# Kernel tuning notes

Hardware: AMD Instinct MI355X
Metric: run time of the kernel (lower is better)

The kernel has to match this reference:

```python
import jax, jax.numpy as jnp
import numpy as np
import math

B, S, D, H = 2, 2048, 1024, 16
HD = D // H
KL_GAMMA = 0.1
EPS = 1e-10


def setup_inputs() -> dict:
    key = jax.random.key(0)
    ks = jax.random.split(key, 12)
    # positive inputs + positive weights keep scores > 0 so log(mean(scores)) is finite
    query = jax.random.uniform(ks[0], (B, S, D), dtype=jnp.float32)
    k_in = jax.random.uniform(ks[1], (B, S, D), dtype=jnp.float32)
    v_in = jax.random.uniform(ks[2], (B, S, D), dtype=jnp.float32)
    def w(k):
        return jax.random.uniform(k, (D, D), dtype=jnp.float32) * 0.002
    b = jnp.full((D,), 1e-3, dtype=jnp.float32)
    return {
        "query": query, "key": k_in, "value": v_in,
        "Wq": w(ks[3]), "bq": b,
        "Wk": w(ks[4]), "bk": b,
        "Wv": w(ks[5]), "bv": b,
        "Wo": w(ks[6]), "bo": b,
    }


def reference(query, key, value, Wq, bq, Wk, bk, Wv, bv, Wo, bo):
    Bq, Sq, _ = query.shape
    Sk = key.shape[1]
    # projections, split heads: [B, H, S, HD]
    Q = (query @ Wq + bq).reshape(Bq, Sq, H, HD).transpose(0, 2, 1, 3)
    K = (key @ Wk + bk).reshape(Bq, Sk, H, HD).transpose(0, 2, 1, 3)
    V = (value @ Wv + bv).reshape(Bq, Sk, H, HD).transpose(0, 2, 1, 3)
    scores = jnp.einsum("bhqd,bhkd->bhqk", Q, K) / math.sqrt(HD)  # [B,H,Sq,Sk]
    # KL bias: row-mean broadcast over keys, then log
    target = jnp.mean(scores, axis=-1, keepdims=True)  # [B,H,Sq,1]
    scores = scores + KL_GAMMA * jnp.log(target + EPS)
    attn = jax.nn.softmax(scores, axis=-1)
    ctx = jnp.einsum("bhqk,bhkd->bhqd", attn, V)
    ctx = ctx.transpose(0, 2, 1, 3).reshape(Bq, Sq, D)
    return ctx @ Wo + bo
```

## Files before the change

### kernel.cpp

```cpp
#include <hip/hip_runtime.h>
#include <hip/hip_bf16.h>
#include <stdint.h>


#define NB 2
#define NS 2048
#define ND 1024
#define NH 16
#define HD 64

typedef short bf16x8 __attribute__((ext_vector_type(8)));
typedef short bf16x4 __attribute__((ext_vector_type(4)));
typedef float f32x4 __attribute__((ext_vector_type(4)));
typedef float f32x16 __attribute__((ext_vector_type(16)));
typedef unsigned int u32x4 __attribute__((ext_vector_type(4)));

static __device__ __forceinline__ short f2bf(float f) {
    uint32_t u = __builtin_bit_cast(uint32_t, f);
    uint32_t r = (u + 0x7fffu + ((u >> 16) & 1u)) >> 16;
    return (short)(uint16_t)r;
}

static __device__ __forceinline__ unsigned int cvtpk(float lo, float hi) {
    unsigned int r;
    asm("v_cvt_pk_bf16_f32 %0, %1, %2" : "=v"(r) : "v"(lo), "v"(hi));
    return r;
}

#if __has_builtin(__builtin_amdgcn_exp2f)
#define EXP2(x) __builtin_amdgcn_exp2f(x)
#else
#define EXP2(x) exp2f(x)
#endif

static __device__ __forceinline__ void plswap(unsigned& a, unsigned& b) {
#if __has_builtin(__builtin_amdgcn_permlane32_swap)
    auto r = __builtin_amdgcn_permlane32_swap(a, b, false, false);
    a = r[0]; b = r[1];
#else
    const int l = (int)(threadIdx.x & 63);
    unsigned bl = __shfl(b, l & 31);
    unsigned ah = __shfl(a, (l & 31) + 32);
    a = (l < 32) ? a : bl;
    b = (l < 32) ? ah : b;
#endif
}

typedef __attribute__((address_space(1))) const unsigned int glob_u32;
typedef __attribute__((address_space(3))) unsigned int lds_u32;
static __device__ __forceinline__ void gload16(const void* g, void* l) {
    __builtin_amdgcn_global_load_lds((glob_u32*)g, (lds_u32*)l, 16, 0, 0);
}

__global__ __launch_bounds__(256) void prep_cast(const float* __restrict__ q,
                                                 const float* __restrict__ k,
                                                 const float* __restrict__ v,
                                                 short* __restrict__ Qo,
                                                 short* __restrict__ Ko,
                                                 short* __restrict__ Vo) {
    const float* src = (blockIdx.z == 0) ? q : (blockIdx.z == 1) ? k : v;
    short* dst = (blockIdx.z == 0) ? Qo : (blockIdx.z == 1) ? Ko : Vo;
    const size_t i = ((size_t)blockIdx.x * 256 + threadIdx.x) * 8;
    f32x4 a = *(const f32x4*)(src + i);
    f32x4 b = *(const f32x4*)(src + i + 4);
    bf16x8 o;
    o[0] = f2bf(a[0]); o[1] = f2bf(a[1]); o[2] = f2bf(a[2]); o[3] = f2bf(a[3]);
    o[4] = f2bf(b[0]); o[5] = f2bf(b[1]); o[6] = f2bf(b[2]); o[7] = f2bf(b[3]);
    *(bf16x8*)(dst + i) = o;
}

__global__ __launch_bounds__(256) void prep_wt(const float* __restrict__ W0,
                                               const float* __restrict__ W1,
                                               const float* __restrict__ W2,
                                               const float* __restrict__ W3,
                                               short* __restrict__ WtAll) {
    __shared__ short tile[32][33];
    const float* W = (blockIdx.z == 0) ? W0 : (blockIdx.z == 1) ? W1
                   : (blockIdx.z == 2) ? W2 : W3;
    short* Wt = WtAll + (size_t)blockIdx.z * (ND * ND);
    const int tx = threadIdx.x & 31;
    const int ty = threadIdx.x >> 5;
    const int k0 = blockIdx.x * 32, n0 = blockIdx.y * 32;
#pragma unroll
    for (int i = 0; i < 4; i++)
        tile[ty + i * 8][tx] = f2bf(W[(size_t)(k0 + ty + i * 8) * ND + n0 + tx]);
    __syncthreads();
#pragma unroll
    for (int i = 0; i < 4; i++)
        Wt[(size_t)(n0 + ty + i * 8) * ND + k0 + tx] = tile[tx][ty + i * 8];
}

static __device__ __forceinline__ void gemm_body(const short* __restrict__ A,
                                                 const short* __restrict__ Wt,
                                                 const float* __restrict__ bias,
                                                 void* __restrict__ Out,
                                                 int mode, float scale,
                                                 short* As, short* Bs) {
    const int tid = threadIdx.x;
    const int gm = blockIdx.x * 128;
    const int gn = blockIdx.y * 128;
    const int w = tid >> 6;
    const int l = tid & 63;
    const int r = l & 15;
    const int g = l >> 4;
    const int wr = w >> 1, wc = w & 1;

    f32x4 acc[4][4];
#pragma unroll
    for (int m = 0; m < 4; m++)
#pragma unroll
        for (int n = 0; n < 4; n++) acc[m][n] = (f32x4){0.f, 0.f, 0.f, 0.f};

    for (int k0 = 0; k0 < ND; k0 += 32) {
#pragma unroll
        for (int j = 0; j < 2; j++) {
            const int lin = ((w * 2 + j) << 10) + l * 16;
            const int row = lin >> 6;
            const int cb = lin & 63;
            gload16((const char*)A + ((size_t)(gm + row) * ND + k0) * 2 + cb,
                    (char*)As + ((w * 2 + j) << 10));
            gload16((const char*)Wt + ((size_t)(gn + row) * ND + k0) * 2 + cb,
                    (char*)Bs + ((w * 2 + j) << 10));
        }
        __syncthreads();

        bf16x8 af[4], bfv[4];
#pragma unroll
        for (int m = 0; m < 4; m++)
            af[m] = *(const bf16x8*)((const char*)As + (wr * 64 + m * 16 + r) * 64 + g * 16);
#pragma unroll
        for (int n = 0; n < 4; n++)
            bfv[n] = *(const bf16x8*)((const char*)Bs + (wc * 64 + n * 16 + r) * 64 + g * 16);
#pragma unroll
        for (int m = 0; m < 4; m++)
#pragma unroll
            for (int n = 0; n < 4; n++)
                acc[m][n] = __builtin_amdgcn_mfma_f32_16x16x32_bf16(
                    af[m], bfv[n], acc[m][n], 0, 0, 0);
        __syncthreads();
    }

#pragma unroll
    for (int m = 0; m < 4; m++) {
        const int orow = gm + wr * 64 + m * 16 + g * 4;
#pragma unroll
        for (int n = 0; n < 4; n++) {
            const int ocol = gn + wc * 64 + n * 16 + r;
            const float bv = bias[ocol];
#pragma unroll
            for (int i = 0; i < 4; i++) {
                const float vout = (acc[m][n][i] + bv) * scale;
                const int row = orow + i;
                if (mode == 0) {
                    const int b = row >> 11, s = row & 2047;
                    const int h = ocol >> 6, hd = ocol & 63;
                    ((short*)Out)[(((size_t)(b * NH + h) * NS + s) << 6) + hd] = f2bf(vout);
                } else if (mode == 1) {
                    const int b = row >> 11, s = row & 2047;
                    const int h = ocol >> 6, hd = ocol & 63;
                    ((short*)Out)[((size_t)(b * NH + h) * HD + hd) * NS + s] = f2bf(vout);
                } else {
                    ((float*)Out)[(size_t)row * ND + ocol] = vout;
                }
            }
        }
    }
}

#define QSCALE 0.18033688011112042f

__global__ __launch_bounds__(256, 3) void gemm_qkv(const short* __restrict__ Qin,
                                                   const short* __restrict__ Kin,
                                                   const short* __restrict__ Vin,
                                                   const short* __restrict__ WtAll,
                                                   const float* __restrict__ bq,
                                                   const float* __restrict__ bk,
                                                   const float* __restrict__ bv,
                                                   short* __restrict__ Qo,
                                                   short* __restrict__ Ko,
                                                   short* __restrict__ Vto) {
    __shared__ __align__(16) short As[128 * 32];
    __shared__ __align__(16) short Bs[128 * 32];
    const int z = blockIdx.z;
    const short* A = (z == 0) ? Qin : (z == 1) ? Kin : Vin;
    const short* Wt = WtAll + (size_t)z * ND * ND;
    const float* bias = (z == 0) ? bq : (z == 1) ? bk : bv;
    void* Out = (z == 0) ? (void*)Qo : (z == 1) ? (void*)Ko : (void*)Vto;
    const float scale = (z == 0) ? QSCALE : 1.0f;
    const int mode = (z == 2) ? 1 : 0;
    gemm_body(A, Wt, bias, Out, mode, scale, As, Bs);
}

__global__ __launch_bounds__(256, 3) void gemm_fin(const short* __restrict__ Ctx,
                                                   const short* __restrict__ Wt,
                                                   const float* __restrict__ bo,
                                                   float* __restrict__ Out) {
    __shared__ __align__(16) short As[128 * 32];
    __shared__ __align__(16) short Bs[128 * 32];
    gemm_body(Ctx, Wt, bo, Out, 2, 1.0f, As, Bs);
}

static __device__ __forceinline__ void stage2(const char* Kp8, const char* Vp8,
                                              char* Kbuf, char* Vbuf,
                                              int t, int w, int l) {
#pragma unroll
    for (int jj = 0; jj < 2; jj++) {
        const int chunk = w * 2 + jj;
        const int half = chunk >> 3;
        const int lin = ((chunk & 7) << 10) + l * 16;
        const int sw = lin ^ (((lin >> 7) & 7) << 4);
        const int row = sw >> 7, col = sw & 127;
        gload16(Kp8 + (size_t)(half * 1024 + t * 64 + row) * 128 + col,
                Kbuf + half * 8192 + ((chunk & 7) << 10));
        gload16(Vp8 + (size_t)row * (NS * 2) + (half * 1024 + t * 64) * 2 + col,
                Vbuf + half * 8192 + ((chunk & 7) << 10));
    }
}

__global__ __launch_bounds__(512, 4) void attn_kern(const short* __restrict__ Q,
                                                    const short* __restrict__ K,
                                                    const short* __restrict__ Vt,
                                                    short* __restrict__ Ctx) {
    __shared__ __align__(16) char smem[2][2][16384];

    const int tid = threadIdx.x;
    const int w = tid >> 6;
    const int l = tid & 63;
    const int c = l & 31;
    const int h = l >> 5;
    const int h16 = h << 4;

    const int bid = blockIdx.x;
    const int swb = (bid & 7) * 64 + (bid >> 3);
    const int bh = swb >> 4;
    const int qt = swb & 15;
    const int qb = qt * 128 + (w & 3) * 32;

    const short* Qp = Q + (size_t)bh * NS * HD;
    const char* Kp8 = (const char*)(K + (size_t)bh * NS * HD);
    const char* Vp8 = (const char*)(Vt + (size_t)bh * HD * NS);

    bf16x8 qf[4];
    {
        const short* Qrow = Qp + (size_t)(qb + c) * HD;
#pragma unroll
        for (int st = 0; st < 4; st++)
            qf[st] = *(const bf16x8*)(Qrow + st * 16 + h * 8);
    }

    f32x16 acc[2];
    acc[0] = (f32x16)(0.f);
    acc[1] = (f32x16)(0.f);
    float rsum = 0.f;

    const int khalf = w >> 2;
    const int sx = (c & 7) << 4;

    stage2(Kp8, Vp8, smem[0][0], smem[0][1], 0, w, l);
    __syncthreads();

    int bufi = 0;
    for (int t = 0; t < 16; t++) {
        if (t < 15)
            stage2(Kp8, Vp8, smem[bufi ^ 1][0], smem[bufi ^ 1][1], t + 1, w, l);

        const char* Kt = smem[bufi][0] + khalf * 8192;
        const char* Vv = smem[bufi][1] + khalf * 8192;

#pragma unroll
        for (int ktile = 0; ktile < 2; ktile++) {
            bf16x8 kf[4];
#pragma unroll
            for (int st = 0; st < 4; st++)
                kf[st] = *(const bf16x8*)(Kt + ((ktile * 32 + c) << 7) +
                                          ((st * 32 + h16) ^ sx));
            f32x16 S = (f32x16)(0.f);
#pragma unroll
            for (int st = 0; st < 4; st++)
                S = __builtin_amdgcn_mfma_f32_32x32x16_bf16(kf[st], qf[st], S, 0, 0, 0);

            float tv[16];
#pragma unroll
            for (int i = 0; i < 16; i++) { tv[i] = EXP2(S[i]); rsum += tv[i]; }

            unsigned v0[4], v1[4];
#pragma unroll
            for (int q4 = 0; q4 < 4; q4++) {
                v0[q4] = cvtpk(tv[4 * q4], tv[4 * q4 + 1]);
                v1[q4] = cvtpk(tv[4 * q4 + 2], tv[4 * q4 + 3]);
            }

#pragma unroll
            for (int ks = 0; ks < 2; ks++) {
                unsigned a0 = v0[2 * ks], b0 = v0[2 * ks + 1];
                unsigned a1 = v1[2 * ks], b1 = v1[2 * ks + 1];
                plswap(a0, b0);
                plswap(a1, b1);
                u32x4 paw; paw[0] = a0; paw[1] = a1; paw[2] = b0; paw[3] = b1;
                bf16x8 pa = __builtin_bit_cast(bf16x8, paw);
#pragma unroll
                for (int dt = 0; dt < 2; dt++) {
                    bf16x8 vb = *(const bf16x8*)(Vv + ((dt * 32 + c) << 7) +
                                                 ((ktile * 64 + ks * 32 + h16) ^ sx));
                    acc[dt] = __builtin_amdgcn_mfma_f32_32x32x16_bf16(pa, vb, acc[dt], 0, 0, 0);
                }
            }
        }
        __syncthreads();
        bufi ^= 1;
    }

    rsum += __shfl_xor(rsum, 32);

    float* rsbuf = (float*)&smem[0][0][0];
    float* sumbuf = (float*)&smem[0][0][0] + 256;
    if (h == 0) rsbuf[w * 32 + c] = rsum;
    if (w >= 4) {
#pragma unroll
        for (int q4 = 0; q4 < 4; q4++)
#pragma unroll
            for (int i = 0; i < 4; i++) {
                const int qrow = i + 8 * q4 + 4 * h;
#pragma unroll
                for (int dt = 0; dt < 2; dt++)
                    sumbuf[(((w - 4) * 32 + qrow) << 6) + dt * 32 + c] = acc[dt][q4 * 4 + i];
            }
    }
    __syncthreads();
    if (w < 4) {
        const int b = bh >> 4, hh = bh & 15;
#pragma unroll
        for (int q4 = 0; q4 < 4; q4++)
#pragma unroll
            for (int i = 0; i < 4; i++) {
                const int qrow = i + 8 * q4 + 4 * h;
                const float inv = 1.0f / (rsbuf[w * 32 + qrow] + rsbuf[(w + 4) * 32 + qrow]);
                short* op = Ctx + ((size_t)b * NS + qb + qrow) * ND + hh * HD;
#pragma unroll
                for (int dt = 0; dt < 2; dt++) {
                    const float vsum = acc[dt][q4 * 4 + i] +
                                       sumbuf[((w * 32 + qrow) << 6) + dt * 32 + c];
                    op[dt * 32 + c] = f2bf(vsum * inv);
                }
            }
    }
}

extern "C" void kernel_launch(void* const* d_in, const int* in_sizes, int n_in,
                              void* d_out, int out_size, void* d_ws, size_t ws_size,
                              hipStream_t stream) {
    (void)in_sizes; (void)n_in; (void)out_size; (void)ws_size;
    const float* query = (const float*)d_in[0];
    const float* key_  = (const float*)d_in[1];
    const float* value = (const float*)d_in[2];
    const float* Wq = (const float*)d_in[3];
    const float* bq = (const float*)d_in[4];
    const float* Wk = (const float*)d_in[5];
    const float* bk = (const float*)d_in[6];
    const float* Wv = (const float*)d_in[7];
    const float* bv = (const float*)d_in[8];
    const float* Wo = (const float*)d_in[9];
    const float* bo = (const float*)d_in[10];

    char* ws = (char*)d_ws;
    const size_t MB = 1024 * 1024;
    short* WtAll = (short*)ws;
    short* Qin = (short*)(ws + 8 * MB);
    short* Kin = (short*)(ws + 16 * MB);
    short* Vin = (short*)(ws + 24 * MB);
    short* Qb  = (short*)(ws + 32 * MB);
    short* Kb  = (short*)(ws + 40 * MB);
    short* Vtb = (short*)(ws + 48 * MB);
    short* Ctx = (short*)(ws + 8 * MB);

    prep_cast<<<dim3(2048, 1, 3), 256, 0, stream>>>(query, key_, value, Qin, Kin, Vin);
    prep_wt<<<dim3(32, 32, 4), 256, 0, stream>>>(Wq, Wk, Wv, Wo, WtAll);
    gemm_qkv<<<dim3(32, 8, 3), 256, 0, stream>>>(Qin, Kin, Vin, WtAll, bq, bk, bv,
                                                 Qb, Kb, Vtb);
    attn_kern<<<dim3(512), 512, 0, stream>>>(Qb, Kb, Vtb, Ctx);
    gemm_fin<<<dim3(32, 8), 256, 0, stream>>>(Ctx, WtAll + 3 * ND * ND, bo, (float*)d_out);
}
```

Measured before the change: 119.3 us.

## Double-buffer GEMM LDS tiles and XOR-swizzle them to avoid bank conflicts

The shared projection GEMM body now keeps two LDS stages per operand. It prefetches the next K-slice from global memory while MFMAs run on the current one, which removes one barrier per iteration and hides load latency. Tile columns are XOR-swizzled by row on both the store and fragment-read sides to reduce LDS bank conflicts on the bf16x8 reads. LDS use per block doubles, which may limit how many blocks fit on a CU under the 3-blocks launch bound.

```diff
diff --git a/kernel.cpp b/kernel.cpp
--- a/kernel.cpp
+++ b/kernel.cpp
@@ -95,7 +95,7 @@
                                                  const float* __restrict__ bias,
                                                  void* __restrict__ Out,
                                                  int mode, float scale,
-                                                 short* As, short* Bs) {
+                                                 char* As2, char* Bs2) {
     const int tid = threadIdx.x;
     const int gm = blockIdx.x * 128;
     const int gn = blockIdx.y * 128;
@@ -111,26 +111,47 @@
 #pragma unroll
         for (int n = 0; n < 4; n++) acc[m][n] = (f32x4){0.f, 0.f, 0.f, 0.f};
 
-    for (int k0 = 0; k0 < ND; k0 += 32) {
-#pragma unroll
-        for (int j = 0; j < 2; j++) {
-            const int lin = ((w * 2 + j) << 10) + l * 16;
-            const int row = lin >> 6;
-            const int cb = lin & 63;
-            gload16((const char*)A + ((size_t)(gm + row) * ND + k0) * 2 + cb,
-                    (char*)As + ((w * 2 + j) << 10));
-            gload16((const char*)Wt + ((size_t)(gn + row) * ND + k0) * 2 + cb,
-                    (char*)Bs + ((w * 2 + j) << 10));
+    const int lin = ((w * 2) << 10) + l * 16;
+#pragma unroll
+    for (int j = 0; j < 2; j++) {
+        const int lj = lin + (j << 10);
+        const int row = lj >> 6;
+        const int colL = (lj & 63) ^ (((row ^ (row >> 2)) & 3) << 4);
+        gload16((const char*)A + (size_t)(gm + row) * (ND * 2) + colL, As2 + lj);
+        gload16((const char*)Wt + (size_t)(gn + row) * (ND * 2) + colL, Bs2 + lj);
+    }
+    __syncthreads();
+
+    for (int t = 0; t < ND / 32; t++) {
+        const int cur = (t & 1) << 13;
+        const int nxt = cur ^ 8192;
+        if (t < ND / 32 - 1) {
+            const int k0b = (t + 1) * 64;
+#pragma unroll
+            for (int j = 0; j < 2; j++) {
+                const int lj = lin + (j << 10);
+                const int row = lj >> 6;
+                const int colL = (lj & 63) ^ (((row ^ (row >> 2)) & 3) << 4);
+                gload16((const char*)A + (size_t)(gm + row) * (ND * 2) + k0b + colL,
+                        As2 + nxt + lj);
+                gload16((const char*)Wt + (size_t)(gn + row) * (ND * 2) + k0b + colL,
+                        Bs2 + nxt + lj);
+            }
         }
-        __syncthreads();
 
         bf16x8 af[4], bfv[4];
 #pragma unroll
-        for (int m = 0; m < 4; m++)
-            af[m] = *(const bf16x8*)((const char*)As + (wr * 64 + m * 16 + r) * 64 + g * 16);
-#pragma unroll
-        for (int n = 0; n < 4; n++)
-            bfv[n] = *(const bf16x8*)((const char*)Bs + (wc * 64 + n * 16 + r) * 64 + g * 16);
+        for (int m = 0; m < 4; m++) {
+            const int ar = wr * 64 + m * 16 + r;
+            const int fa = ((ar ^ (ar >> 2)) & 3) << 4;
+            af[m] = *(const bf16x8*)(As2 + cur + ar * 64 + ((g << 4) ^ fa));
+        }
+#pragma unroll
+        for (int n = 0; n < 4; n++) {
+            const int br = wc * 64 + n * 16 + r;
+            const int fb = ((br ^ (br >> 2)) & 3) << 4;
+            bfv[n] = *(const bf16x8*)(Bs2 + cur + br * 64 + ((g << 4) ^ fb));
+        }
 #pragma unroll
         for (int m = 0; m < 4; m++)
 #pragma unroll
@@ -179,8 +200,8 @@
                                                    short* __restrict__ Qo,
                                                    short* __restrict__ Ko,
                                                    short* __restrict__ Vto) {
-    __shared__ __align__(16) short As[128 * 32];
-    __shared__ __align__(16) short Bs[128 * 32];
+    __shared__ __align__(16) char As[2 * 8192];
+    __shared__ __align__(16) char Bs[2 * 8192];
     const int z = blockIdx.z;
     const short* A = (z == 0) ? Qin : (z == 1) ? Kin : Vin;
     const short* Wt = WtAll + (size_t)z * ND * ND;
@@ -195,8 +216,8 @@
                                                    const short* __restrict__ Wt,
                                                    const float* __restrict__ bo,
                                                    float* __restrict__ Out) {
-    __shared__ __align__(16) short As[128 * 32];
-    __shared__ __align__(16) short Bs[128 * 32];
+    __shared__ __align__(16) char As[2 * 8192];
+    __shared__ __align__(16) char Bs[2 * 8192];
     gemm_body(Ctx, Wt, bo, Out, 2, 1.0f, As, Bs);
 }
 
```

New measurement: 119.1 us. About the same (-0.2%).
